# Performance work log

Hardware: AMD Instinct MI355X
Metric: run time of the kernel (lower is better)

The kernel has to match this reference:

```python
import jax, jax.numpy as jnp
import numpy as np

B, M, D = 2048, 40, 16
LAYERS = [128, 128, 128]


def setup_inputs() -> dict:
    key = jax.random.key(0)
    ks = jax.random.split(key, 8)
    s = 0.05
    x = jax.random.normal(ks[0], (B, M, D), jnp.float32)
    w0 = jax.random.normal(ks[1], (128, M * M), jnp.float32) * s      # in = n_dim*n_dim = 1600
    b0 = jax.random.normal(ks[2], (128,), jnp.float32) * s
    w1 = jax.random.normal(ks[3], (128, 64 * M), jnp.float32) * s     # prev halved to 64 -> in = 2560
    b1 = jax.random.normal(ks[4], (128,), jnp.float32) * s
    w2 = jax.random.normal(ks[5], (128, 64 * M), jnp.float32) * s
    b2 = jax.random.normal(ks[6], (128,), jnp.float32) * s
    wl = jax.random.normal(ks[7], (1, 64 * 3), jnp.float32) * s       # n_feat_map = 64+64+64
    return {"x": x, "w0": w0, "b0": b0, "w1": w1, "b1": b1,
            "w2": w2, "b2": b2, "wl": wl}


def reference(x, w0, b0, w1, b1, w2, b2, wl):
    # x: [B, M, D]; CIN with half_split=True and all-even layers.
    _, m, _ = x.shape
    prev = x
    direct = []
    for w, b in ((w0, b0), (w1, b1), (w2, b2)):
        h = prev.shape[1]
        o = w.shape[0]
        wr = w.reshape(o, h, m)
        # Fused outer-product + 1x1 conv:
        # einsum('bhd,bmd->bhmd') reshaped to [B, h*m, D] then conv1d(k=1)
        out = jnp.einsum('bhd,bmd,ohm->bod', prev, x, wr) + b[None, :, None]
        out = jax.nn.relu(out)
        half = o // 2
        prev = out[:, :half]          # next hidden
        direct.append(out[:, half:])  # direct connection
    feat = jnp.concatenate(direct, axis=1).sum(-1)  # [B, n_feat_map]
    return feat @ wl.T  # [B, 1]
```

## Files before the change

kernel.cpp:

```cpp
#include <hip/hip_runtime.h>
#include <hip/hip_bf16.h>

typedef _Float16 f16x8 __attribute__((ext_vector_type(8)));
typedef float f32x4   __attribute__((ext_vector_type(4)));
typedef float f32x16  __attribute__((ext_vector_type(16)));

__device__ __forceinline__ unsigned cvt2h(float a, float b) {
  auto h = __builtin_amdgcn_cvt_pkrtz(a, b);
  unsigned u; __builtin_memcpy(&u, &h, 4); return u;
}

__device__ __forceinline__ f32x16 MFMA(uint4 a, uint4 b, f32x16 c) {
  return __builtin_amdgcn_mfma_f32_32x32x16_f16(
      __builtin_bit_cast(f16x8, a), __builtin_bit_cast(f16x8, b), c, 0, 0, 0);
}

__device__ __forceinline__ int xp_idx(int n, int h) { return (n << 6) + (h ^ ((n & 15) << 2)); }

__global__ __launch_bounds__(256) void permute_w_kernel(
    const float* __restrict__ w0, const float* __restrict__ w1,
    const float* __restrict__ w2, unsigned short* __restrict__ Wp) {
  __shared__ float rowt[40 * 65];
  const int b = blockIdx.x;
  const float* src; unsigned short* dst; int Kin, L0, o;
  if (b < 128)      { o = b;       src = w0 + o * 1600; dst = Wp;          Kin = 1600; L0 = 1; }
  else if (b < 256) { o = b - 128; src = w1 + o * 2560; dst = Wp + 327680; Kin = 2560; L0 = 0; }
  else              { o = b - 256; src = w2 + o * 2560; dst = Wp + 655360; Kin = 2560; L0 = 0; }
  for (int i = threadIdx.x; i < (Kin >> 2); i += 256) {
    float4 v = ((const float4*)src)[i];
    int f = i << 2;
    int h = f / 40, m = f - h * 40;
    rowt[(m + 0) * 65 + h] = v.x;
    rowt[(m + 1) * 65 + h] = v.y;
    rowt[(m + 2) * 65 + h] = v.z;
    rowt[(m + 3) * 65 + h] = v.w;
  }
  __syncthreads();
  const int ot = o >> 5, lanelo = o & 31;
  for (int i = threadIdx.x; i < 320; i += 256) {
    const int k = i << 3;
    const int m = k >> 6, h = k & 63;
    const int s = k >> 4, hi2 = (k >> 3) & 1;
    uint4 u;
    if (L0 && h >= 40) {
      u = make_uint4(0u, 0u, 0u, 0u);
    } else {
      const float* p = &rowt[m * 65 + h];
      u.x = cvt2h(p[0], p[1]); u.y = cvt2h(p[2], p[3]);
      u.z = cvt2h(p[4], p[5]); u.w = cvt2h(p[6], p[7]);
    }
    *(uint4*)&dst[(((size_t)ot * 160 + s) * 64 + lanelo + hi2 * 32) * 8] = u;
  }
}

__global__ __launch_bounds__(1024, 1) void cin_kernel(
    const float* __restrict__ x, const unsigned short* __restrict__ Wp,
    const float* __restrict__ bias0, const float* __restrict__ bias1,
    const float* __restrict__ bias2, const float* __restrict__ wl,
    float* __restrict__ out) {
  __shared__ __align__(16) float XP_s[128 * 64];
  __shared__ __align__(16) unsigned XT_u[40 * 128];
  __shared__ __align__(16) float scr_s[16384];
  __shared__ float wl_s[192];
  __shared__ float s_s[128];

  const int tid = threadIdx.x;
  const int lane = tid & 63;
  const int wv = tid >> 6;
  const int bid = blockIdx.x;
  const int l31 = lane & 31;
  const int hi = lane >> 5;
  const int ki = wv & 3;
  const int oq = wv >> 2;

  if (tid < 192) wl_s[tid] = wl[tid];
  if (tid < 128) s_s[tid] = 0.f;

  {
    const float4* xg = (const float4*)(x + (size_t)bid * 5120);
    for (int i = tid; i < 1280; i += 1024) {
      float4 v = xg[i];
      int d4 = (i & 3) << 2;
      int m = (i >> 2) % 40;
      int b_l = i / 160;
      int nb = b_l * 16 + d4;
      XP_s[xp_idx(nb + 0, m)] = v.x;
      XP_s[xp_idx(nb + 1, m)] = v.y;
      XP_s[xp_idx(nb + 2, m)] = v.z;
      XP_s[xp_idx(nb + 3, m)] = v.w;
      uint4 u;
      u.x = cvt2h(v.x, v.x); u.y = cvt2h(v.y, v.y);
      u.z = cvt2h(v.z, v.z); u.w = cvt2h(v.w, v.w);
      *(uint4*)&XT_u[(m << 7) + nb] = u;
    }
    if (tid < 768) {
      int n = tid / 6, hg = 40 + (tid - n * 6) * 4;
      *(float4*)&XP_s[xp_idx(n, hg)] = make_float4(0.f, 0.f, 0.f, 0.f);
    }
  }
  __syncthreads();

  const int hq = ki * 16 + hi * 8;
  float sacc[4] = {0.f, 0.f, 0.f, 0.f};
  const float* biasL[3] = {bias0, bias1, bias2};

  for (int lidx = 0; lidx < 3; ++lidx) {
    const unsigned short* W = Wp + (size_t)lidx * 327680;
    const float* bias = biasL[lidx];

    f32x16 acc[4];
#pragma unroll
    for (int f = 0; f < 4; ++f)
#pragma unroll
      for (int e = 0; e < 16; ++e) acc[f][e] = 0.f;

    if (!(lidx == 0 && ki == 3)) {
      uint4 Pc[4];
#pragma unroll
      for (int fn = 0; fn < 4; ++fn) {
        const int col = fn * 32 + l31;
        const int rb = col << 6, sw = (col & 15) << 2;
        f32x4 pa = *(const f32x4*)&XP_s[rb + (hq ^ sw)];
        f32x4 pb = *(const f32x4*)&XP_s[rb + ((hq + 4) ^ sw)];
        Pc[fn].x = cvt2h(pa[0], pa[1]); Pc[fn].y = cvt2h(pa[2], pa[3]);
        Pc[fn].z = cvt2h(pb[0], pb[1]); Pc[fn].w = cvt2h(pb[2], pb[3]);
      }
      const unsigned short* wp = W + (((size_t)(oq * 160 + ki)) << 9) + (lane << 3);
      uint4 Aa = *(const uint4*)wp;
      uint4 Ab;
      for (int t = 0; t < 40; t += 2) {
        Ab = *(const uint4*)(wp + (t + 1) * 2048);
#pragma unroll
        for (int fn = 0; fn < 4; ++fn) {
          unsigned xu = XT_u[(t << 7) + fn * 32 + l31];
          uint4 Bu;
          asm("v_pk_mul_f16 %0, %1, %2" : "=v"(Bu.x) : "v"(Pc[fn].x), "v"(xu));
          asm("v_pk_mul_f16 %0, %1, %2" : "=v"(Bu.y) : "v"(Pc[fn].y), "v"(xu));
          asm("v_pk_mul_f16 %0, %1, %2" : "=v"(Bu.z) : "v"(Pc[fn].z), "v"(xu));
          asm("v_pk_mul_f16 %0, %1, %2" : "=v"(Bu.w) : "v"(Pc[fn].w), "v"(xu));
          acc[fn] = MFMA(Aa, Bu, acc[fn]);
        }
        Aa = *(const uint4*)(wp + ((t + 2 < 40) ? (t + 2) : 0) * 2048);
#pragma unroll
        for (int fn = 0; fn < 4; ++fn) {
          unsigned xu = XT_u[((t + 1) << 7) + fn * 32 + l31];
          uint4 Bu;
          asm("v_pk_mul_f16 %0, %1, %2" : "=v"(Bu.x) : "v"(Pc[fn].x), "v"(xu));
          asm("v_pk_mul_f16 %0, %1, %2" : "=v"(Bu.y) : "v"(Pc[fn].y), "v"(xu));
          asm("v_pk_mul_f16 %0, %1, %2" : "=v"(Bu.z) : "v"(Pc[fn].z), "v"(xu));
          asm("v_pk_mul_f16 %0, %1, %2" : "=v"(Bu.w) : "v"(Pc[fn].w), "v"(xu));
          acc[fn] = MFMA(Ab, Bu, acc[fn]);
        }
      }
    }

    __syncthreads();
#pragma unroll
    for (int fp = 0; fp < 2; ++fp) {
      if (ki >= 2) {
        const int base = ((oq << 1) | (ki - 2)) << 11;
#pragma unroll
        for (int fl = 0; fl < 2; ++fl)
#pragma unroll
          for (int qd = 0; qd < 4; ++qd) {
            const int f = fp * 2 + fl;
            f32x4 v = {acc[f][qd*4+0], acc[f][qd*4+1], acc[f][qd*4+2], acc[f][qd*4+3]};
            *(f32x4*)&scr_s[base + ((fl << 2) | qd) * 256 + (lane << 2)] = v;
          }
      }
      __syncthreads();
      if (ki < 2) {
        const int base = ((oq << 1) | ki) << 11;
#pragma unroll
        for (int fl = 0; fl < 2; ++fl)
#pragma unroll
          for (int qd = 0; qd < 4; ++qd) {
            const int f = fp * 2 + fl;
            f32x4 v = *(const f32x4*)&scr_s[base + ((fl << 2) | qd) * 256 + (lane << 2)];
#pragma unroll
            for (int r = 0; r < 4; ++r) acc[f][qd * 4 + r] += v[r];
          }
      }
      __syncthreads();
    }
    if (ki == 1) {
      const int base = oq << 12;
#pragma unroll
      for (int f = 0; f < 4; ++f)
#pragma unroll
        for (int qd = 0; qd < 4; ++qd) {
          f32x4 v = {acc[f][qd*4+0], acc[f][qd*4+1], acc[f][qd*4+2], acc[f][qd*4+3]};
          *(f32x4*)&scr_s[base + ((f << 2) | qd) * 256 + (lane << 2)] = v;
        }
    }
    __syncthreads();
    if (ki == 0) {
      const int base = oq << 12;
#pragma unroll
      for (int f = 0; f < 4; ++f)
#pragma unroll
        for (int qd = 0; qd < 4; ++qd) {
          f32x4 v = *(const f32x4*)&scr_s[base + ((f << 2) | qd) * 256 + (lane << 2)];
#pragma unroll
          for (int r = 0; r < 4; ++r) acc[f][qd * 4 + r] += v[r];
        }
      if (oq < 2) {
        if (lidx < 2) {
#pragma unroll
          for (int fn = 0; fn < 4; ++fn) {
            const int col = fn * 32 + l31;
            const int rb = col << 6, sw = (col & 15) << 2;
#pragma unroll
            for (int qd = 0; qd < 4; ++qd) {
              const int o0 = oq * 32 + qd * 8 + hi * 4;
              float4 bv = *(const float4*)&bias[o0];
              f32x4 r;
              r[0] = fmaxf(acc[fn][qd*4+0] + bv.x, 0.f);
              r[1] = fmaxf(acc[fn][qd*4+1] + bv.y, 0.f);
              r[2] = fmaxf(acc[fn][qd*4+2] + bv.z, 0.f);
              r[3] = fmaxf(acc[fn][qd*4+3] + bv.w, 0.f);
              *(f32x4*)&XP_s[rb + (o0 ^ sw)] = r;
            }
          }
        }
      } else {
#pragma unroll
        for (int fn = 0; fn < 4; ++fn)
#pragma unroll
          for (int qd = 0; qd < 4; ++qd) {
            const int o0 = 64 + (oq - 2) * 32 + qd * 8 + hi * 4;
            float4 bv = *(const float4*)&bias[o0];
            float4 wv4 = *(const float4*)&wl_s[lidx * 64 + (o0 - 64)];
            sacc[fn] += fmaxf(acc[fn][qd*4+0] + bv.x, 0.f) * wv4.x
                      + fmaxf(acc[fn][qd*4+1] + bv.y, 0.f) * wv4.y
                      + fmaxf(acc[fn][qd*4+2] + bv.z, 0.f) * wv4.z
                      + fmaxf(acc[fn][qd*4+3] + bv.w, 0.f) * wv4.w;
          }
      }
    }
    __syncthreads();
  }

#pragma unroll
  for (int f = 0; f < 4; ++f) {
    float v = sacc[f] + __shfl_xor(sacc[f], 32);
    if (ki == 0 && oq >= 2 && lane < 32) atomicAdd(&s_s[f * 32 + l31], v);
  }
  __syncthreads();
  if (tid < 8) {
    float s = 0.f;
#pragma unroll
    for (int d = 0; d < 16; ++d) s += s_s[tid * 16 + d];
    out[bid * 8 + tid] = s;
  }
}

extern "C" void kernel_launch(void* const* d_in, const int* in_sizes, int n_in,
                              void* d_out, int out_size, void* d_ws, size_t ws_size,
                              hipStream_t stream) {
  const float* x  = (const float*)d_in[0];
  const float* w0 = (const float*)d_in[1];
  const float* b0 = (const float*)d_in[2];
  const float* w1 = (const float*)d_in[3];
  const float* b1 = (const float*)d_in[4];
  const float* w2 = (const float*)d_in[5];
  const float* b2 = (const float*)d_in[6];
  const float* wl = (const float*)d_in[7];
  unsigned short* Wp = (unsigned short*)d_ws;

  permute_w_kernel<<<384, 256, 0, stream>>>(w0, w1, w2, Wp);
  cin_kernel<<<256, 1024, 0, stream>>>(x, Wp, b0, b1, b2, wl, (float*)d_out);
}
```

Before: 137.0 us.

## Halve block size and give each wave two output row tiles sharing B operands

The CIN kernel moves from 1024 to 512 threads per block. Each wave now computes two 32-row output tiles (acc[2][4]), so the B fragments built with packed f16 multiplies are reused across two MFMAs. The weight prefetch is deepened to two steps, and the split-K reduction through shared memory is restructured to match. The atomicAdd accumulation is replaced by direct stores because each output slot now has a single writer. Doubling the accumulators raises register pressure, and with only 256 blocks and launch bounds of (512,2) the GPU may be underfilled.

```diff
diff --git a/kernel.cpp b/kernel.cpp
--- a/kernel.cpp
+++ b/kernel.cpp
@@ -53,7 +53,7 @@
   }
 }
 
-__global__ __launch_bounds__(1024, 1) void cin_kernel(
+__global__ __launch_bounds__(512, 2) void cin_kernel(
     const float* __restrict__ x, const unsigned short* __restrict__ Wp,
     const float* __restrict__ bias0, const float* __restrict__ bias1,
     const float* __restrict__ bias2, const float* __restrict__ wl,
@@ -71,14 +71,13 @@
   const int l31 = lane & 31;
   const int hi = lane >> 5;
   const int ki = wv & 3;
-  const int oq = wv >> 2;
+  const int oh = wv >> 2;
 
   if (tid < 192) wl_s[tid] = wl[tid];
-  if (tid < 128) s_s[tid] = 0.f;
 
   {
     const float4* xg = (const float4*)(x + (size_t)bid * 5120);
-    for (int i = tid; i < 1280; i += 1024) {
+    for (int i = tid; i < 1280; i += 512) {
       float4 v = xg[i];
       int d4 = (i & 3) << 2;
       int m = (i >> 2) % 40;
@@ -93,8 +92,8 @@
       u.z = cvt2h(v.z, v.z); u.w = cvt2h(v.w, v.w);
       *(uint4*)&XT_u[(m << 7) + nb] = u;
     }
-    if (tid < 768) {
-      int n = tid / 6, hg = 40 + (tid - n * 6) * 4;
+    for (int i = tid; i < 768; i += 512) {
+      int n = i / 6, hg = 40 + (i - n * 6) * 4;
       *(float4*)&XP_s[xp_idx(n, hg)] = make_float4(0.f, 0.f, 0.f, 0.f);
     }
   }
@@ -108,11 +107,13 @@
     const unsigned short* W = Wp + (size_t)lidx * 327680;
     const float* bias = biasL[lidx];
 
-    f32x16 acc[4];
-#pragma unroll
-    for (int f = 0; f < 4; ++f)
-#pragma unroll
-      for (int e = 0; e < 16; ++e) acc[f][e] = 0.f;
+    f32x16 acc[2][4];
+#pragma unroll
+    for (int mr = 0; mr < 2; ++mr)
+#pragma unroll
+      for (int f = 0; f < 4; ++f)
+#pragma unroll
+        for (int e = 0; e < 16; ++e) acc[mr][f][e] = 0.f;
 
     if (!(lidx == 0 && ki == 3)) {
       uint4 Pc[4];
@@ -125,11 +126,16 @@
         Pc[fn].x = cvt2h(pa[0], pa[1]); Pc[fn].y = cvt2h(pa[2], pa[3]);
         Pc[fn].z = cvt2h(pb[0], pb[1]); Pc[fn].w = cvt2h(pb[2], pb[3]);
       }
-      const unsigned short* wp = W + (((size_t)(oq * 160 + ki)) << 9) + (lane << 3);
-      uint4 Aa = *(const uint4*)wp;
-      uint4 Ab;
+      const unsigned short* wp0 = W + (((size_t)((oh * 2 + 0) * 160 + ki)) << 9) + (lane << 3);
+      const unsigned short* wp1 = W + (((size_t)((oh * 2 + 1) * 160 + ki)) << 9) + (lane << 3);
+      auto ldf = [&](const unsigned short* p, int t) -> uint4 {
+        return *(const uint4*)(p + (t < 40 ? t : 0) * 2048);
+      };
+      uint4 Aa0 = ldf(wp0, 0), Aa1 = ldf(wp1, 0);
+      uint4 Ab0 = ldf(wp0, 1), Ab1 = ldf(wp1, 1);
+#pragma unroll
       for (int t = 0; t < 40; t += 2) {
-        Ab = *(const uint4*)(wp + (t + 1) * 2048);
+        uint4 Ac0 = ldf(wp0, t + 2), Ac1 = ldf(wp1, t + 2);
 #pragma unroll
         for (int fn = 0; fn < 4; ++fn) {
           unsigned xu = XT_u[(t << 7) + fn * 32 + l31];
@@ -138,9 +144,10 @@
           asm("v_pk_mul_f16 %0, %1, %2" : "=v"(Bu.y) : "v"(Pc[fn].y), "v"(xu));
           asm("v_pk_mul_f16 %0, %1, %2" : "=v"(Bu.z) : "v"(Pc[fn].z), "v"(xu));
           asm("v_pk_mul_f16 %0, %1, %2" : "=v"(Bu.w) : "v"(Pc[fn].w), "v"(xu));
-          acc[fn] = MFMA(Aa, Bu, acc[fn]);
+          acc[0][fn] = MFMA(Aa0, Bu, acc[0][fn]);
+          acc[1][fn] = MFMA(Aa1, Bu, acc[1][fn]);
         }
-        Aa = *(const uint4*)(wp + ((t + 2 < 40) ? (t + 2) : 0) * 2048);
+        uint4 Ad0 = ldf(wp0, t + 3), Ad1 = ldf(wp1, t + 3);
 #pragma unroll
         for (int fn = 0; fn < 4; ++fn) {
           unsigned xu = XT_u[((t + 1) << 7) + fn * 32 + l31];
@@ -149,93 +156,101 @@
           asm("v_pk_mul_f16 %0, %1, %2" : "=v"(Bu.y) : "v"(Pc[fn].y), "v"(xu));
           asm("v_pk_mul_f16 %0, %1, %2" : "=v"(Bu.z) : "v"(Pc[fn].z), "v"(xu));
           asm("v_pk_mul_f16 %0, %1, %2" : "=v"(Bu.w) : "v"(Pc[fn].w), "v"(xu));
-          acc[fn] = MFMA(Ab, Bu, acc[fn]);
+          acc[0][fn] = MFMA(Ab0, Bu, acc[0][fn]);
+          acc[1][fn] = MFMA(Ab1, Bu, acc[1][fn]);
         }
+        Aa0 = Ac0; Aa1 = Ac1; Ab0 = Ad0; Ab1 = Ad1;
       }
     }
 
     __syncthreads();
 #pragma unroll
-    for (int fp = 0; fp < 2; ++fp) {
+    for (int mr = 0; mr < 2; ++mr) {
       if (ki >= 2) {
-        const int base = ((oq << 1) | (ki - 2)) << 11;
-#pragma unroll
-        for (int fl = 0; fl < 2; ++fl)
-#pragma unroll
-          for (int qd = 0; qd < 4; ++qd) {
-            const int f = fp * 2 + fl;
-            f32x4 v = {acc[f][qd*4+0], acc[f][qd*4+1], acc[f][qd*4+2], acc[f][qd*4+3]};
-            *(f32x4*)&scr_s[base + ((fl << 2) | qd) * 256 + (lane << 2)] = v;
+        const int base = ((oh << 1) | (ki - 2)) << 12;
+#pragma unroll
+        for (int f = 0; f < 4; ++f)
+#pragma unroll
+          for (int qd = 0; qd < 4; ++qd) {
+            f32x4 v = {acc[mr][f][qd*4+0], acc[mr][f][qd*4+1], acc[mr][f][qd*4+2], acc[mr][f][qd*4+3]};
+            *(f32x4*)&scr_s[base + ((f << 2) | qd) * 256 + (lane << 2)] = v;
           }
       }
       __syncthreads();
       if (ki < 2) {
-        const int base = ((oq << 1) | ki) << 11;
-#pragma unroll
-        for (int fl = 0; fl < 2; ++fl)
-#pragma unroll
-          for (int qd = 0; qd < 4; ++qd) {
-            const int f = fp * 2 + fl;
-            f32x4 v = *(const f32x4*)&scr_s[base + ((fl << 2) | qd) * 256 + (lane << 2)];
-#pragma unroll
-            for (int r = 0; r < 4; ++r) acc[f][qd * 4 + r] += v[r];
+        const int base = ((oh << 1) | ki) << 12;
+#pragma unroll
+        for (int f = 0; f < 4; ++f)
+#pragma unroll
+          for (int qd = 0; qd < 4; ++qd) {
+            f32x4 v = *(const f32x4*)&scr_s[base + ((f << 2) | qd) * 256 + (lane << 2)];
+#pragma unroll
+            for (int r = 0; r < 4; ++r) acc[mr][f][qd * 4 + r] += v[r];
           }
       }
       __syncthreads();
     }
     if (ki == 1) {
-      const int base = oq << 12;
-#pragma unroll
-      for (int f = 0; f < 4; ++f)
-#pragma unroll
-        for (int qd = 0; qd < 4; ++qd) {
-          f32x4 v = {acc[f][qd*4+0], acc[f][qd*4+1], acc[f][qd*4+2], acc[f][qd*4+3]};
-          *(f32x4*)&scr_s[base + ((f << 2) | qd) * 256 + (lane << 2)] = v;
-        }
+      const int base = oh << 13;
+#pragma unroll
+      for (int mr = 0; mr < 2; ++mr)
+#pragma unroll
+        for (int f = 0; f < 4; ++f)
+#pragma unroll
+          for (int qd = 0; qd < 4; ++qd) {
+            f32x4 v = {acc[mr][f][qd*4+0], acc[mr][f][qd*4+1], acc[mr][f][qd*4+2], acc[mr][f][qd*4+3]};
+            *(f32x4*)&scr_s[base + (((mr << 2) | f) << 2 | qd) * 256 + (lane << 2)] = v;
+          }
     }
     __syncthreads();
     if (ki == 0) {
-      const int base = oq << 12;
-#pragma unroll
-      for (int f = 0; f < 4; ++f)
-#pragma unroll
-        for (int qd = 0; qd < 4; ++qd) {
-          f32x4 v = *(const f32x4*)&scr_s[base + ((f << 2) | qd) * 256 + (lane << 2)];
-#pragma unroll
-          for (int r = 0; r < 4; ++r) acc[f][qd * 4 + r] += v[r];
-        }
-      if (oq < 2) {
+      const int base = oh << 13;
+#pragma unroll
+      for (int mr = 0; mr < 2; ++mr)
+#pragma unroll
+        for (int f = 0; f < 4; ++f)
+#pragma unroll
+          for (int qd = 0; qd < 4; ++qd) {
+            f32x4 v = *(const f32x4*)&scr_s[base + (((mr << 2) | f) << 2 | qd) * 256 + (lane << 2)];
+#pragma unroll
+            for (int r = 0; r < 4; ++r) acc[mr][f][qd * 4 + r] += v[r];
+          }
+      if (oh == 0) {
         if (lidx < 2) {
 #pragma unroll
-          for (int fn = 0; fn < 4; ++fn) {
-            const int col = fn * 32 + l31;
-            const int rb = col << 6, sw = (col & 15) << 2;
-#pragma unroll
-            for (int qd = 0; qd < 4; ++qd) {
-              const int o0 = oq * 32 + qd * 8 + hi * 4;
-              float4 bv = *(const float4*)&bias[o0];
-              f32x4 r;
-              r[0] = fmaxf(acc[fn][qd*4+0] + bv.x, 0.f);
-              r[1] = fmaxf(acc[fn][qd*4+1] + bv.y, 0.f);
-              r[2] = fmaxf(acc[fn][qd*4+2] + bv.z, 0.f);
-              r[3] = fmaxf(acc[fn][qd*4+3] + bv.w, 0.f);
-              *(f32x4*)&XP_s[rb + (o0 ^ sw)] = r;
+          for (int mr = 0; mr < 2; ++mr)
+#pragma unroll
+            for (int fn = 0; fn < 4; ++fn) {
+              const int col = fn * 32 + l31;
+              const int rb = col << 6, sw = (col & 15) << 2;
+#pragma unroll
+              for (int qd = 0; qd < 4; ++qd) {
+                const int o0 = mr * 32 + qd * 8 + hi * 4;
+                float4 bv = *(const float4*)&bias[o0];
+                f32x4 r;
+                r[0] = fmaxf(acc[mr][fn][qd*4+0] + bv.x, 0.f);
+                r[1] = fmaxf(acc[mr][fn][qd*4+1] + bv.y, 0.f);
+                r[2] = fmaxf(acc[mr][fn][qd*4+2] + bv.z, 0.f);
+                r[3] = fmaxf(acc[mr][fn][qd*4+3] + bv.w, 0.f);
+                *(f32x4*)&XP_s[rb + (o0 ^ sw)] = r;
+              }
             }
-          }
         }
       } else {
 #pragma unroll
-        for (int fn = 0; fn < 4; ++fn)
-#pragma unroll
-          for (int qd = 0; qd < 4; ++qd) {
-            const int o0 = 64 + (oq - 2) * 32 + qd * 8 + hi * 4;
-            float4 bv = *(const float4*)&bias[o0];
-            float4 wv4 = *(const float4*)&wl_s[lidx * 64 + (o0 - 64)];
-            sacc[fn] += fmaxf(acc[fn][qd*4+0] + bv.x, 0.f) * wv4.x
-                      + fmaxf(acc[fn][qd*4+1] + bv.y, 0.f) * wv4.y
-                      + fmaxf(acc[fn][qd*4+2] + bv.z, 0.f) * wv4.z
-                      + fmaxf(acc[fn][qd*4+3] + bv.w, 0.f) * wv4.w;
-          }
+        for (int mr = 0; mr < 2; ++mr)
+#pragma unroll
+          for (int fn = 0; fn < 4; ++fn)
+#pragma unroll
+            for (int qd = 0; qd < 4; ++qd) {
+              const int o0 = 64 + mr * 32 + qd * 8 + hi * 4;
+              float4 bv = *(const float4*)&bias[o0];
+              float4 wv4 = *(const float4*)&wl_s[lidx * 64 + (o0 - 64)];
+              sacc[fn] += fmaxf(acc[mr][fn][qd*4+0] + bv.x, 0.f) * wv4.x
+                        + fmaxf(acc[mr][fn][qd*4+1] + bv.y, 0.f) * wv4.y
+                        + fmaxf(acc[mr][fn][qd*4+2] + bv.z, 0.f) * wv4.z
+                        + fmaxf(acc[mr][fn][qd*4+3] + bv.w, 0.f) * wv4.w;
+            }
       }
     }
     __syncthreads();
@@ -244,7 +259,7 @@
 #pragma unroll
   for (int f = 0; f < 4; ++f) {
     float v = sacc[f] + __shfl_xor(sacc[f], 32);
-    if (ki == 0 && oq >= 2 && lane < 32) atomicAdd(&s_s[f * 32 + l31], v);
+    if (ki == 0 && oh == 1 && lane < 32) s_s[f * 32 + l31] = v;
   }
   __syncthreads();
   if (tid < 8) {
@@ -269,5 +284,5 @@
   unsigned short* Wp = (unsigned short*)d_ws;
 
   permute_w_kernel<<<384, 256, 0, stream>>>(w0, w1, w2, Wp);
-  cin_kernel<<<256, 1024, 0, stream>>>(x, Wp, b0, b1, b2, wl, (float*)d_out);
-}
+  cin_kernel<<<256, 512, 0, stream>>>(x, Wp, b0, b1, b2, wl, (float*)d_out);
+}
```

After: 133.0 us. -3.0%, faster.
